# Kernel optimization log

Hardware: AMD Instinct MI355X
Metric: run time of the kernel (lower is better)

The kernel has to match this reference:

```python
import math
import jax
import jax.numpy as jnp
import numpy as np

B = 4096        # number of contexts / segments
T = 262144      # total objects across all segments (avg 64 per segment)
F = 128         # object_size
H = 256         # hidden_size
C = 512         # context_size


def setup_inputs() -> dict:
    key = jax.random.key(0)
    ks = jax.random.split(key, 8)
    objects = jax.random.normal(ks[0], (T, F), dtype=jnp.float32)
    context = jax.random.normal(ks[1], (B, C), dtype=jnp.float32)
    # sorted segment ids; guarantee every segment non-empty by seeding one id per segment
    extra = jax.random.randint(ks[2], (T - B,), 0, B)
    segment_ids = jnp.sort(jnp.concatenate([jnp.arange(B, dtype=extra.dtype), extra])).astype(jnp.int32)
    s = 0.05
    return {
        "objects": objects,
        "context": context,
        "segment_ids": segment_ids,
        "W1": jax.random.normal(ks[3], (F, H), dtype=jnp.float32) * s,
        "b1": jnp.zeros((H,), dtype=jnp.float32),
        "W2": jax.random.normal(ks[4], (H, H), dtype=jnp.float32) * s,
        "b2": jnp.zeros((H,), dtype=jnp.float32),
        "W3": jax.random.normal(ks[5], (H, 2 * H), dtype=jnp.float32) * s,
        "b3": jnp.zeros((2 * H,), dtype=jnp.float32),
        "Wq": jax.random.normal(ks[6], (C, H), dtype=jnp.float32) * s,
        "bq": jnp.zeros((H,), dtype=jnp.float32),
    }


def reference(objects, context, segment_ids, W1, b1, W2, b2, W3, b3, Wq, bq):
    num_segments = context.shape[0]
    # kv MLP: Linear -> ReLU -> Linear -> ReLU -> Linear(2H)
    h = jax.nn.relu(objects @ W1 + b1)
    h = jax.nn.relu(h @ W2 + b2)
    kv = h @ W3 + b3                                   # [T, 2H]
    k, v = jnp.split(kv, 2, axis=1)                    # [T, H] each
    # query per object via repeat_interleave == gather by segment id
    q = (context @ Wq + bq)[segment_ids]               # [T, H]
    logits = jnp.sum(q * k, axis=1) / math.sqrt(k.shape[1])   # [T]
    # per-segment stable softmax
    m = jax.ops.segment_max(logits, segment_ids, num_segments=num_segments)
    e = jnp.exp(logits - m[segment_ids])
    z = jax.ops.segment_sum(e, segment_ids, num_segments=num_segments)
    w = e / z[segment_ids]                             # [T]
    # per-segment weighted sum of values
    embedding = jax.ops.segment_sum(w[:, None] * v, segment_ids, num_segments=num_segments)  # [B, H]
    return embedding, w
```

## Files before the change

kernel.cpp:

```cpp
#include <hip/hip_runtime.h>
#include <hip/hip_bf16.h>

#define T_TOTAL 262144
#define B_SEG   4096

typedef __attribute__((ext_vector_type(8))) short short8;
typedef __attribute__((ext_vector_type(4))) float f32x4;

__device__ __forceinline__ short f2bf(float x) {
    __hip_bfloat16 h = __float2bfloat16(x);
    return *reinterpret_cast<short*>(&h);
}
__device__ __forceinline__ float bf2f(short s) {
    unsigned u = ((unsigned)(unsigned short)s) << 16;
    return __uint_as_float(u);
}

__global__ __launch_bounds__(256) void transpose_weights(
    const float* __restrict__ W1, const float* __restrict__ W2,
    const float* __restrict__ W3,
    short* __restrict__ W1T, short* __restrict__ W2T, short* __restrict__ W3vT) {
    __shared__ float t[64][68];
    const int b = blockIdx.x, tid = threadIdx.x;
    const float* src; short* dst;
    int k0, n0_src, n0_dst, sstride, dstride;
    if (b < 8) {
        int kt = b >> 2, nt = b & 3;
        src = W1; dst = W1T; sstride = 256; dstride = 128;
        k0 = kt * 64; n0_src = nt * 64; n0_dst = nt * 64;
    } else if (b < 24) {
        int id = b - 8, kt = id >> 2, nt = id & 3;
        src = W2; dst = W2T; sstride = 256; dstride = 256;
        k0 = kt * 64; n0_src = nt * 64; n0_dst = nt * 64;
    } else {
        int id = b - 24, kt = id >> 2, nt = id & 3;
        src = W3; dst = W3vT; sstride = 512; dstride = 256;
        k0 = kt * 64; n0_src = 256 + nt * 64; n0_dst = nt * 64;
    }
    {
        int r = tid >> 4, c4 = (tid & 15) * 4;
#pragma unroll
        for (int p = 0; p < 4; p++) {
            int k = p * 16 + r;
            float4 v = *reinterpret_cast<const float4*>(&src[(size_t)(k0 + k) * sstride + n0_src + c4]);
            *reinterpret_cast<float4*>(&t[k][c4]) = v;
        }
    }
    __syncthreads();
    {
        int n = tid >> 2, kq = tid & 3;
        short8 s0, s1;
#pragma unroll
        for (int i = 0; i < 8; i++) s0[i] = f2bf(t[kq * 16 + i][n]);
#pragma unroll
        for (int i = 0; i < 8; i++) s1[i] = f2bf(t[kq * 16 + 8 + i][n]);
        short* o = &dst[(size_t)(n0_dst + n) * dstride + k0 + kq * 16];
        *reinterpret_cast<short8*>(o) = s0;
        *reinterpret_cast<short8*>(o + 8) = s1;
    }
}

__global__ __launch_bounds__(256) void vec_kernel(
    const float* __restrict__ Wq, const float* __restrict__ W3,
    const float* __restrict__ bq, const float* __restrict__ b3,
    float* __restrict__ bz, float* __restrict__ wc, float* __restrict__ c0) {
    const int tid = threadIdx.x;
    if (blockIdx.x == 0) {
        float s = 0.f;
        for (int n = 0; n < 256; n += 4) {
            float4 a = *reinterpret_cast<const float4*>(&W3[(size_t)tid * 512 + n]);
            float4 b = *reinterpret_cast<const float4*>(&bq[n]);
            s += a.x * b.x + a.y * b.y + a.z * b.z + a.w * b.w;
        }
        bz[tid] = s;
    } else {
#pragma unroll
        for (int h = 0; h < 2; h++) {
            int c = h * 256 + tid;
            float s = 0.f;
            for (int n = 0; n < 256; n += 4) {
                float4 a = *reinterpret_cast<const float4*>(&Wq[(size_t)c * 256 + n]);
                float4 b = *reinterpret_cast<const float4*>(&b3[n]);
                s += a.x * b.x + a.y * b.y + a.z * b.z + a.w * b.w;
            }
            wc[c] = s;
        }
        if (tid == 0) {
            float s = 0.f;
            for (int n = 0; n < 256; n++) s += bq[n] * b3[n];
            c0[0] = s;
        }
    }
}

__global__ __launch_bounds__(256) void prep_wqz(
    const float* __restrict__ Wq, const float* __restrict__ W3,
    float* __restrict__ Wqz) {
    __shared__ float wq[16][260];
    __shared__ float w3[16][260];
    const int tid = threadIdx.x;
    const int c0 = (blockIdx.x >> 4) * 16, j0 = (blockIdx.x & 15) * 16;
    {
        int r = tid >> 4, nq = tid & 15;
#pragma unroll
        for (int p = 0; p < 4; p++) {
            int col = nq * 4 + p * 64;
            *reinterpret_cast<float4*>(&wq[r][col]) =
                *reinterpret_cast<const float4*>(&Wq[(size_t)(c0 + r) * 256 + col]);
            *reinterpret_cast<float4*>(&w3[r][col]) =
                *reinterpret_cast<const float4*>(&W3[(size_t)(j0 + r) * 512 + col]);
        }
    }
    __syncthreads();
    const int ci = tid >> 4, ji = tid & 15;
    float s = 0.f;
    for (int n = 0; n < 256; n += 4) {
        float4 a = *reinterpret_cast<const float4*>(&wq[ci][n]);
        float4 b = *reinterpret_cast<const float4*>(&w3[ji][n]);
        s += a.x * b.x + a.y * b.y + a.z * b.z + a.w * b.w;
    }
    Wqz[(size_t)(c0 + ci) * 256 + j0 + ji] = s;
}

__global__ __launch_bounds__(256) void zq_kernel(
    const float* __restrict__ ctx, const float* __restrict__ Wqz,
    const float* __restrict__ bz, float* __restrict__ zq) {
    __shared__ float As[2][16][68];
    const int tid = threadIdx.x;
    const int tm = tid & 15, tn = tid >> 4;
    const int row0 = blockIdx.x * 64, col0 = blockIdx.y * 64;
    const int lr = tid >> 2, lk = tid & 3;

    float acc[4][4];
#pragma unroll
    for (int i = 0; i < 4; i++)
#pragma unroll
        for (int j = 0; j < 4; j++) acc[i][j] = 0.f;

    float4 av = *reinterpret_cast<const float4*>(&ctx[(size_t)(row0 + lr) * 512 + lk * 4]);
    for (int c = 0; c < 32; c++) {
        int cur = c & 1;
        As[cur][lk * 4 + 0][lr] = av.x;
        As[cur][lk * 4 + 1][lr] = av.y;
        As[cur][lk * 4 + 2][lr] = av.z;
        As[cur][lk * 4 + 3][lr] = av.w;
        __syncthreads();
        if (c < 31)
            av = *reinterpret_cast<const float4*>(
                &ctx[(size_t)(row0 + lr) * 512 + (c + 1) * 16 + lk * 4]);
#pragma unroll
        for (int k = 0; k < 16; k++) {
            float4 a = *reinterpret_cast<const float4*>(&As[cur][k][tm * 4]);
            float4 b = *reinterpret_cast<const float4*>(
                &Wqz[(size_t)(c * 16 + k) * 256 + col0 + tn * 4]);
#pragma unroll
            for (int i = 0; i < 4; i++) {
                float ai = (i == 0) ? a.x : (i == 1) ? a.y : (i == 2) ? a.z : a.w;
                acc[i][0] += ai * b.x; acc[i][1] += ai * b.y;
                acc[i][2] += ai * b.z; acc[i][3] += ai * b.w;
            }
        }
    }
    float4 bv = *reinterpret_cast<const float4*>(&bz[col0 + tn * 4]);
#pragma unroll
    for (int i = 0; i < 4; i++) {
        float4 o = {acc[i][0] + bv.x, acc[i][1] + bv.y, acc[i][2] + bv.z, acc[i][3] + bv.w};
        *reinterpret_cast<float4*>(&zq[(size_t)(row0 + tm * 4 + i) * 256 + col0 + tn * 4]) = o;
    }
}

__global__ __launch_bounds__(256) void cvec_kernel(
    const float* __restrict__ ctx, const float* __restrict__ wc,
    const float* __restrict__ c0, float* __restrict__ cbuf) {
    const int tid = threadIdx.x;
    const int row = blockIdx.x * 32 + (tid >> 3);
    const int l = tid & 7;
    float s = 0.f;
    for (int i = 0; i < 64; i += 4) {
        float4 a = *reinterpret_cast<const float4*>(&ctx[(size_t)row * 512 + l * 64 + i]);
        float4 b = *reinterpret_cast<const float4*>(&wc[l * 64 + i]);
        s += a.x * b.x + a.y * b.y + a.z * b.z + a.w * b.w;
    }
    s += __shfl_xor(s, 1); s += __shfl_xor(s, 2); s += __shfl_xor(s, 4);
    if (l == 0) cbuf[row] = s + c0[0];
}

template <int K>
__device__ __forceinline__ void run_layer(
    const short* __restrict__ act, const short* __restrict__ Wt,
    int mbase, int nbase, int l16, int quad, f32x4 acc[4][4]) {
    constexpr int KK = K / 32;
    const f32x4 zero = {0.f, 0.f, 0.f, 0.f};
#pragma unroll
    for (int i = 0; i < 4; i++)
#pragma unroll
        for (int j = 0; j < 4; j++) acc[i][j] = zero;

    int woff[4];
#pragma unroll
    for (int ns = 0; ns < 4; ns++)
        woff[ns] = ((nbase + ns * 16 + l16) * K + quad * 8) * 2;
    const int abase = (mbase + l16) * K * 2;
    const char* actc = reinterpret_cast<const char*>(act);
    const char* wtc  = reinterpret_cast<const char*>(Wt);

    short8 wbuf[2][4];
    short8 areg[4];

#pragma unroll
    for (int ns = 0; ns < 4; ns++)
        wbuf[0][ns] = *reinterpret_cast<const short8*>(wtc + woff[ns]);

#pragma unroll
    for (int kk = 0; kk < KK; kk++) {
        if (kk + 1 < KK) {
#pragma unroll
            for (int ns = 0; ns < 4; ns++)
                wbuf[(kk + 1) & 1][ns] = *reinterpret_cast<const short8*>(
                    wtc + woff[ns] + (kk + 1) * 64);
        }
        {
            const int sg = (((kk * 4 + quad) ^ l16) * 16);
#pragma unroll
            for (int ms = 0; ms < 4; ms++)
                areg[ms] = *reinterpret_cast<const short8*>(
                    actc + abase + ms * 16 * K * 2 + sg);
        }
        const int cb = kk & 1;
#pragma unroll
        for (int ms = 0; ms < 4; ms++)
#pragma unroll
            for (int ns = 0; ns < 4; ns++)
                acc[ms][ns] = __builtin_amdgcn_mfma_f32_16x16x32_bf16(
                    wbuf[cb][ns], areg[ms], acc[ms][ns], 0, 0, 0);
    }
}

__global__ __launch_bounds__(512, 4) void mlp_kernel(
    const float* __restrict__ objects, const int* __restrict__ seg_ids,
    const short* __restrict__ W1T, const short* __restrict__ W2T,
    const short* __restrict__ W3vT,
    const float* __restrict__ b1, const float* __restrict__ b2,
    const float* __restrict__ b3,
    const float* __restrict__ zqbuf, const float* __restrict__ cbuf,
    float* __restrict__ logits_out, short* __restrict__ vout) {
    __shared__ __align__(16) short bufH[128 * 256];
    __shared__ float slots[4][128];

    const int tid  = threadIdx.x;
    const int wave = tid >> 6;
    const int lane = tid & 63;
    const int quad = lane >> 4;
    const int l16  = lane & 15;
    const int mbase = (wave & 1) * 64;
    const int wn    = wave >> 1;
    const int nbase = wn * 64;
    const int row0  = blockIdx.x * 128;

    {
        const float4* op = reinterpret_cast<const float4*>(objects + (size_t)row0 * 128);
#pragma unroll
        for (int i = 0; i < 4; i++) {
            int u = tid + i * 512;
            int m = u >> 4, kg = u & 15;
            float4 x0 = op[u * 2];
            float4 x1 = op[u * 2 + 1];
            short8 s;
            s[0] = f2bf(x0.x); s[1] = f2bf(x0.y); s[2] = f2bf(x0.z); s[3] = f2bf(x0.w);
            s[4] = f2bf(x1.x); s[5] = f2bf(x1.y); s[6] = f2bf(x1.z); s[7] = f2bf(x1.w);
            *reinterpret_cast<short8*>(&bufH[m * 128 + ((kg ^ (m & 15)) * 8)]) = s;
        }
    }
    __syncthreads();

    f32x4 acc[4][4];

    auto store_act = [&](const float* __restrict__ bias) {
#pragma unroll
        for (int ns = 0; ns < 4; ns++) {
            int n0 = nbase + ns * 16 + quad * 4;
            float4 bv = *reinterpret_cast<const float4*>(&bias[n0]);
#pragma unroll
            for (int ms = 0; ms < 4; ms++) {
                int m = mbase + ms * 16 + l16;
                short4 s;
                s.x = f2bf(fmaxf(acc[ms][ns][0] + bv.x, 0.f));
                s.y = f2bf(fmaxf(acc[ms][ns][1] + bv.y, 0.f));
                s.z = f2bf(fmaxf(acc[ms][ns][2] + bv.z, 0.f));
                s.w = f2bf(fmaxf(acc[ms][ns][3] + bv.w, 0.f));
                *reinterpret_cast<short4*>(
                    &bufH[m * 256 + (((n0 >> 3) ^ (m & 15)) * 8) + (n0 & 7)]) = s;
            }
        }
    };

    run_layer<128>(bufH, W1T, mbase, nbase, l16, quad, acc);
    __syncthreads();
    store_act(b1);
    __syncthreads();

    run_layer<256>(bufH, W2T, mbase, nbase, l16, quad, acc);
    __syncthreads();
    {
        float part[4] = {0.f, 0.f, 0.f, 0.f};
        int segm[4];
#pragma unroll
        for (int ms = 0; ms < 4; ms++) segm[ms] = seg_ids[row0 + mbase + ms * 16 + l16];
#pragma unroll
        for (int ns = 0; ns < 4; ns++) {
            int n0 = nbase + ns * 16 + quad * 4;
            float4 bv = *reinterpret_cast<const float4*>(&b2[n0]);
#pragma unroll
            for (int ms = 0; ms < 4; ms++) {
                int m = mbase + ms * 16 + l16;
                float h0 = fmaxf(acc[ms][ns][0] + bv.x, 0.f);
                float h1v = fmaxf(acc[ms][ns][1] + bv.y, 0.f);
                float h2v = fmaxf(acc[ms][ns][2] + bv.z, 0.f);
                float h3 = fmaxf(acc[ms][ns][3] + bv.w, 0.f);
                short4 s;
                s.x = f2bf(h0); s.y = f2bf(h1v); s.z = f2bf(h2v); s.w = f2bf(h3);
                *reinterpret_cast<short4*>(
                    &bufH[m * 256 + (((n0 >> 3) ^ (m & 15)) * 8) + (n0 & 7)]) = s;
                float4 zq4 = *reinterpret_cast<const float4*>(
                    &zqbuf[(size_t)segm[ms] * 256 + n0]);
                part[ms] += h0 * zq4.x + h1v * zq4.y + h2v * zq4.z + h3 * zq4.w;
            }
        }
#pragma unroll
        for (int ms = 0; ms < 4; ms++) {
            float p = part[ms];
            p += __shfl_xor(p, 16);
            p += __shfl_xor(p, 32);
            if (quad == 0) slots[wn][mbase + ms * 16 + l16] = p;
        }
    }
    __syncthreads();
    if (tid < 128) {
        int seg = seg_ids[row0 + tid];
        float s = slots[0][tid] + slots[1][tid] + slots[2][tid] + slots[3][tid] + cbuf[seg];
        logits_out[row0 + tid] = s * 0.0625f;
    }

    run_layer<256>(bufH, W3vT, mbase, nbase, l16, quad, acc);
    __syncthreads();
#pragma unroll
    for (int ns = 0; ns < 4; ns++) {
        int n0 = nbase + ns * 16 + quad * 4;
        float4 bv = *reinterpret_cast<const float4*>(&b3[256 + n0]);
#pragma unroll
        for (int ms = 0; ms < 4; ms++) {
            int m = mbase + ms * 16 + l16;
            short4 s;
            s.x = f2bf(acc[ms][ns][0] + bv.x);
            s.y = f2bf(acc[ms][ns][1] + bv.y);
            s.z = f2bf(acc[ms][ns][2] + bv.z);
            s.w = f2bf(acc[ms][ns][3] + bv.w);
            *reinterpret_cast<short4*>(
                &bufH[m * 256 + (((n0 >> 3) ^ (m & 15)) * 8) + (n0 & 7)]) = s;
        }
    }
    __syncthreads();
#pragma unroll
    for (int i = 0; i < 8; i++) {
        int idx = tid + i * 512;
        int m = idx >> 5, sg = idx & 31;
        short8 val = *reinterpret_cast<const short8*>(&bufH[m * 256 + sg * 8]);
        int n0 = (sg ^ (m & 15)) * 8;
        *reinterpret_cast<short8*>(&vout[(size_t)(row0 + m) * 256 + n0]) = val;
    }
}

__global__ __launch_bounds__(256) void segment_kernel(
    const float* __restrict__ logits, const short* __restrict__ vbuf,
    const int* __restrict__ seg_ids, float* __restrict__ emb,
    float* __restrict__ wout) {
    const int b = blockIdx.x;
    const int tid = threadIdx.x;
    __shared__ int range[2];
    __shared__ float wred[4];
    __shared__ float slots[4][256];

    if (tid < 2) {
        int target = b + tid;
        int lo = 0, hi = T_TOTAL;
        while (lo < hi) {
            int mid = (lo + hi) >> 1;
            if (seg_ids[mid] < target) lo = mid + 1; else hi = mid;
        }
        range[tid] = lo;
    }
    __syncthreads();
    const int start = range[0], end = range[1];

    float mx = -1e30f;
    for (int t = start + tid; t < end; t += 256) mx = fmaxf(mx, logits[t]);
#pragma unroll
    for (int off = 32; off >= 1; off >>= 1) mx = fmaxf(mx, __shfl_xor(mx, off));
    if ((tid & 63) == 0) wred[tid >> 6] = mx;
    __syncthreads();
    mx = fmaxf(fmaxf(wred[0], wred[1]), fmaxf(wred[2], wred[3]));
    __syncthreads();

    float s = 0.f;
    for (int t = start + tid; t < end; t += 256) s += __expf(logits[t] - mx);
#pragma unroll
    for (int off = 32; off >= 1; off >>= 1) s += __shfl_xor(s, off);
    if ((tid & 63) == 0) wred[tid >> 6] = s;
    __syncthreads();
    float invz = 1.f / (wred[0] + wred[1] + wred[2] + wred[3]);

    for (int t = start + tid; t < end; t += 256)
        wout[t] = __expf(logits[t] - mx) * invz;

    const int cg = tid & 63, r = tid >> 6;
    float a0 = 0.f, a1 = 0.f, a2 = 0.f, a3 = 0.f;
    for (int t = start + r; t < end; t += 4) {
        float wv = __expf(logits[t] - mx) * invz;
        short4 v4 = *reinterpret_cast<const short4*>(&vbuf[(size_t)t * 256 + cg * 4]);
        a0 += wv * bf2f(v4.x);
        a1 += wv * bf2f(v4.y);
        a2 += wv * bf2f(v4.z);
        a3 += wv * bf2f(v4.w);
    }
    float4 av = {a0, a1, a2, a3};
    *reinterpret_cast<float4*>(&slots[r][cg * 4]) = av;
    __syncthreads();
    emb[(size_t)b * 256 + tid] =
        slots[0][tid] + slots[1][tid] + slots[2][tid] + slots[3][tid];
}

extern "C" void kernel_launch(void* const* d_in, const int* in_sizes, int n_in,
                              void* d_out, int out_size, void* d_ws, size_t ws_size,
                              hipStream_t stream) {
    const float* objects = (const float*)d_in[0];
    const float* context = (const float*)d_in[1];
    const int*   seg     = (const int*)d_in[2];
    const float* W1 = (const float*)d_in[3];
    const float* b1 = (const float*)d_in[4];
    const float* W2 = (const float*)d_in[5];
    const float* b2 = (const float*)d_in[6];
    const float* W3 = (const float*)d_in[7];
    const float* b3 = (const float*)d_in[8];
    const float* Wq = (const float*)d_in[9];
    const float* bq = (const float*)d_in[10];

    char* ws = (char*)d_ws;
    float* zqbuf = (float*)(ws);
    float* cbuf  = (float*)(ws + 4194304);
    short* W1T   = (short*)(ws + 4210688);
    short* W2T   = (short*)(ws + 4276224);
    short* W3vT  = (short*)(ws + 4407296);
    char*  lreg   = ws + 4538368;
    float* logits = (float*)lreg;
    float* Wqz    = (float*)lreg;
    float* bz     = (float*)(lreg + 524288);
    float* wc     = (float*)(lreg + 525312);
    float* c0     = (float*)(lreg + 527360);
    short* vbuf   = (short*)(ws + 5586944);

    float* emb  = (float*)d_out;
    float* wout = emb + (size_t)B_SEG * 256;

    transpose_weights<<<40, 256, 0, stream>>>(W1, W2, W3, W1T, W2T, W3vT);
    vec_kernel<<<2, 256, 0, stream>>>(Wq, W3, bq, b3, bz, wc, c0);
    prep_wqz<<<512, 256, 0, stream>>>(Wq, W3, Wqz);
    zq_kernel<<<dim3(64, 4), 256, 0, stream>>>(context, Wqz, bz, zqbuf);
    cvec_kernel<<<128, 256, 0, stream>>>(context, wc, c0, cbuf);
    mlp_kernel<<<T_TOTAL / 128, 512, 0, stream>>>(objects, seg, W1T, W2T, W3vT,
                                                  b1, b2, b3, zqbuf, cbuf,
                                                  logits, vbuf);
    segment_kernel<<<B_SEG, 256, 0, stream>>>(logits, vbuf, seg, emb, wout);
}
```

Baseline: 486.1 us.

## Shrink MLP tile to 64 rows, precompute segment starts, use one-wave segment reduction

The MLP kernel now processes 64 rows per 256-thread block instead of 128 rows per 512-thread block, halving the LDS buffer so more blocks fit per CU. The activation loads are moved ahead of the weight prefetch. A new kernel computes segment start offsets once, replacing the per-block binary search. The segment kernel becomes a single wave with multiple accumulators, which removes the LDS reductions and barriers. seg_starts reuses the cbuf workspace region, but it is written after mlp_kernel has consumed cbuf, so the ordering is safe.

```diff
diff --git a/kernel.cpp b/kernel.cpp
--- a/kernel.cpp
+++ b/kernel.cpp
@@ -188,7 +188,7 @@
 template <int K>
 __device__ __forceinline__ void run_layer(
     const short* __restrict__ act, const short* __restrict__ Wt,
-    int mbase, int nbase, int l16, int quad, f32x4 acc[4][4]) {
+    int nbase, int l16, int quad, f32x4 acc[4][4]) {
     constexpr int KK = K / 32;
     const f32x4 zero = {0.f, 0.f, 0.f, 0.f};
 #pragma unroll
@@ -200,7 +200,7 @@
 #pragma unroll
     for (int ns = 0; ns < 4; ns++)
         woff[ns] = ((nbase + ns * 16 + l16) * K + quad * 8) * 2;
-    const int abase = (mbase + l16) * K * 2;
+    const int abase = l16 * K * 2;
     const char* actc = reinterpret_cast<const char*>(act);
     const char* wtc  = reinterpret_cast<const char*>(Wt);
 
@@ -213,19 +213,19 @@
 
 #pragma unroll
     for (int kk = 0; kk < KK; kk++) {
+        {
+            const int sg = (((kk * 4 + quad) ^ l16) * 16);
+#pragma unroll
+            for (int ms = 0; ms < 4; ms++)
+                areg[ms] = *reinterpret_cast<const short8*>(
+                    actc + abase + ms * 16 * K * 2 + sg);
+        }
         if (kk + 1 < KK) {
 #pragma unroll
             for (int ns = 0; ns < 4; ns++)
                 wbuf[(kk + 1) & 1][ns] = *reinterpret_cast<const short8*>(
                     wtc + woff[ns] + (kk + 1) * 64);
         }
-        {
-            const int sg = (((kk * 4 + quad) ^ l16) * 16);
-#pragma unroll
-            for (int ms = 0; ms < 4; ms++)
-                areg[ms] = *reinterpret_cast<const short8*>(
-                    actc + abase + ms * 16 * K * 2 + sg);
-        }
         const int cb = kk & 1;
 #pragma unroll
         for (int ms = 0; ms < 4; ms++)
@@ -236,7 +236,7 @@
     }
 }
 
-__global__ __launch_bounds__(512, 4) void mlp_kernel(
+__global__ __launch_bounds__(256, 4) void mlp_kernel(
     const float* __restrict__ objects, const int* __restrict__ seg_ids,
     const short* __restrict__ W1T, const short* __restrict__ W2T,
     const short* __restrict__ W3vT,
@@ -244,24 +244,22 @@
     const float* __restrict__ b3,
     const float* __restrict__ zqbuf, const float* __restrict__ cbuf,
     float* __restrict__ logits_out, short* __restrict__ vout) {
-    __shared__ __align__(16) short bufH[128 * 256];
-    __shared__ float slots[4][128];
+    __shared__ __align__(16) short bufH[64 * 256];
+    __shared__ float slots[4][64];
 
     const int tid  = threadIdx.x;
     const int wave = tid >> 6;
     const int lane = tid & 63;
     const int quad = lane >> 4;
     const int l16  = lane & 15;
-    const int mbase = (wave & 1) * 64;
-    const int wn    = wave >> 1;
-    const int nbase = wn * 64;
-    const int row0  = blockIdx.x * 128;
+    const int nbase = wave * 64;
+    const int row0  = blockIdx.x * 64;
 
     {
         const float4* op = reinterpret_cast<const float4*>(objects + (size_t)row0 * 128);
 #pragma unroll
         for (int i = 0; i < 4; i++) {
-            int u = tid + i * 512;
+            int u = tid + i * 256;
             int m = u >> 4, kg = u & 15;
             float4 x0 = op[u * 2];
             float4 x1 = op[u * 2 + 1];
@@ -282,7 +280,7 @@
             float4 bv = *reinterpret_cast<const float4*>(&bias[n0]);
 #pragma unroll
             for (int ms = 0; ms < 4; ms++) {
-                int m = mbase + ms * 16 + l16;
+                int m = ms * 16 + l16;
                 short4 s;
                 s.x = f2bf(fmaxf(acc[ms][ns][0] + bv.x, 0.f));
                 s.y = f2bf(fmaxf(acc[ms][ns][1] + bv.y, 0.f));
@@ -294,25 +292,25 @@
         }
     };
 
-    run_layer<128>(bufH, W1T, mbase, nbase, l16, quad, acc);
+    run_layer<128>(bufH, W1T, nbase, l16, quad, acc);
     __syncthreads();
     store_act(b1);
     __syncthreads();
 
-    run_layer<256>(bufH, W2T, mbase, nbase, l16, quad, acc);
+    run_layer<256>(bufH, W2T, nbase, l16, quad, acc);
     __syncthreads();
     {
         float part[4] = {0.f, 0.f, 0.f, 0.f};
         int segm[4];
 #pragma unroll
-        for (int ms = 0; ms < 4; ms++) segm[ms] = seg_ids[row0 + mbase + ms * 16 + l16];
+        for (int ms = 0; ms < 4; ms++) segm[ms] = seg_ids[row0 + ms * 16 + l16];
 #pragma unroll
         for (int ns = 0; ns < 4; ns++) {
             int n0 = nbase + ns * 16 + quad * 4;
             float4 bv = *reinterpret_cast<const float4*>(&b2[n0]);
 #pragma unroll
             for (int ms = 0; ms < 4; ms++) {
-                int m = mbase + ms * 16 + l16;
+                int m = ms * 16 + l16;
                 float h0 = fmaxf(acc[ms][ns][0] + bv.x, 0.f);
                 float h1v = fmaxf(acc[ms][ns][1] + bv.y, 0.f);
                 float h2v = fmaxf(acc[ms][ns][2] + bv.z, 0.f);
@@ -331,17 +329,17 @@
             float p = part[ms];
             p += __shfl_xor(p, 16);
             p += __shfl_xor(p, 32);
-            if (quad == 0) slots[wn][mbase + ms * 16 + l16] = p;
-        }
-    }
-    __syncthreads();
-    if (tid < 128) {
+            if (quad == 0) slots[wave][ms * 16 + l16] = p;
+        }
+    }
+    __syncthreads();
+    if (tid < 64) {
         int seg = seg_ids[row0 + tid];
         float s = slots[0][tid] + slots[1][tid] + slots[2][tid] + slots[3][tid] + cbuf[seg];
         logits_out[row0 + tid] = s * 0.0625f;
     }
 
-    run_layer<256>(bufH, W3vT, mbase, nbase, l16, quad, acc);
+    run_layer<256>(bufH, W3vT, nbase, l16, quad, acc);
     __syncthreads();
 #pragma unroll
     for (int ns = 0; ns < 4; ns++) {
@@ -349,7 +347,7 @@
         float4 bv = *reinterpret_cast<const float4*>(&b3[256 + n0]);
 #pragma unroll
         for (int ms = 0; ms < 4; ms++) {
-            int m = mbase + ms * 16 + l16;
+            int m = ms * 16 + l16;
             short4 s;
             s.x = f2bf(acc[ms][ns][0] + bv.x);
             s.y = f2bf(acc[ms][ns][1] + bv.y);
@@ -362,7 +360,7 @@
     __syncthreads();
 #pragma unroll
     for (int i = 0; i < 8; i++) {
-        int idx = tid + i * 512;
+        int idx = tid + i * 256;
         int m = idx >> 5, sg = idx & 31;
         short8 val = *reinterpret_cast<const short8*>(&bufH[m * 256 + sg * 8]);
         int n0 = (sg ^ (m & 15)) * 8;
@@ -370,63 +368,76 @@
     }
 }
 
-__global__ __launch_bounds__(256) void segment_kernel(
+__global__ __launch_bounds__(256) void seg_starts_kernel(
+    const int* __restrict__ seg, int* __restrict__ starts) {
+    int t = blockIdx.x * 256 + threadIdx.x;
+    if (t >= T_TOTAL) return;
+    int s = seg[t];
+    if (t == 0) {
+        for (int q = 0; q <= s; q++) starts[q] = 0;
+    } else {
+        int p = seg[t - 1];
+        for (int q = p + 1; q <= s; q++) starts[q] = t;
+    }
+}
+
+__global__ __launch_bounds__(64) void segment_kernel(
     const float* __restrict__ logits, const short* __restrict__ vbuf,
-    const int* __restrict__ seg_ids, float* __restrict__ emb,
+    const int* __restrict__ starts, float* __restrict__ emb,
     float* __restrict__ wout) {
     const int b = blockIdx.x;
-    const int tid = threadIdx.x;
-    __shared__ int range[2];
-    __shared__ float wred[4];
-    __shared__ float slots[4][256];
-
-    if (tid < 2) {
-        int target = b + tid;
-        int lo = 0, hi = T_TOTAL;
-        while (lo < hi) {
-            int mid = (lo + hi) >> 1;
-            if (seg_ids[mid] < target) lo = mid + 1; else hi = mid;
-        }
-        range[tid] = lo;
-    }
-    __syncthreads();
-    const int start = range[0], end = range[1];
+    const int lane = threadIdx.x;
+    const int start = starts[b];
+    const int end = (b == B_SEG - 1) ? T_TOTAL : starts[b + 1];
 
     float mx = -1e30f;
-    for (int t = start + tid; t < end; t += 256) mx = fmaxf(mx, logits[t]);
+    for (int t = start + lane; t < end; t += 64) mx = fmaxf(mx, logits[t]);
 #pragma unroll
     for (int off = 32; off >= 1; off >>= 1) mx = fmaxf(mx, __shfl_xor(mx, off));
-    if ((tid & 63) == 0) wred[tid >> 6] = mx;
-    __syncthreads();
-    mx = fmaxf(fmaxf(wred[0], wred[1]), fmaxf(wred[2], wred[3]));
-    __syncthreads();
 
     float s = 0.f;
-    for (int t = start + tid; t < end; t += 256) s += __expf(logits[t] - mx);
+    for (int t = start + lane; t < end; t += 64) s += __expf(logits[t] - mx);
 #pragma unroll
     for (int off = 32; off >= 1; off >>= 1) s += __shfl_xor(s, off);
-    if ((tid & 63) == 0) wred[tid >> 6] = s;
-    __syncthreads();
-    float invz = 1.f / (wred[0] + wred[1] + wred[2] + wred[3]);
-
-    for (int t = start + tid; t < end; t += 256)
+    const float invz = 1.f / s;
+
+    for (int t = start + lane; t < end; t += 64)
         wout[t] = __expf(logits[t] - mx) * invz;
 
-    const int cg = tid & 63, r = tid >> 6;
-    float a0 = 0.f, a1 = 0.f, a2 = 0.f, a3 = 0.f;
-    for (int t = start + r; t < end; t += 4) {
+    float a[4][4];
+#pragma unroll
+    for (int i = 0; i < 4; i++)
+#pragma unroll
+        for (int j = 0; j < 4; j++) a[i][j] = 0.f;
+
+    int t = start;
+    for (; t + 8 <= end; t += 8) {
+#pragma unroll
+        for (int u = 0; u < 8; u++) {
+            float wv = __expf(logits[t + u] - mx) * invz;
+            short4 v4 = *reinterpret_cast<const short4*>(
+                &vbuf[(size_t)(t + u) * 256 + lane * 4]);
+            a[u & 3][0] += wv * bf2f(v4.x);
+            a[u & 3][1] += wv * bf2f(v4.y);
+            a[u & 3][2] += wv * bf2f(v4.z);
+            a[u & 3][3] += wv * bf2f(v4.w);
+        }
+    }
+    for (; t < end; t++) {
         float wv = __expf(logits[t] - mx) * invz;
-        short4 v4 = *reinterpret_cast<const short4*>(&vbuf[(size_t)t * 256 + cg * 4]);
-        a0 += wv * bf2f(v4.x);
-        a1 += wv * bf2f(v4.y);
-        a2 += wv * bf2f(v4.z);
-        a3 += wv * bf2f(v4.w);
-    }
-    float4 av = {a0, a1, a2, a3};
-    *reinterpret_cast<float4*>(&slots[r][cg * 4]) = av;
-    __syncthreads();
-    emb[(size_t)b * 256 + tid] =
-        slots[0][tid] + slots[1][tid] + slots[2][tid] + slots[3][tid];
+        short4 v4 = *reinterpret_cast<const short4*>(
+            &vbuf[(size_t)t * 256 + lane * 4]);
+        a[0][0] += wv * bf2f(v4.x);
+        a[0][1] += wv * bf2f(v4.y);
+        a[0][2] += wv * bf2f(v4.z);
+        a[0][3] += wv * bf2f(v4.w);
+    }
+    float4 o;
+    o.x = a[0][0] + a[1][0] + a[2][0] + a[3][0];
+    o.y = a[0][1] + a[1][1] + a[2][1] + a[3][1];
+    o.z = a[0][2] + a[1][2] + a[2][2] + a[3][2];
+    o.w = a[0][3] + a[1][3] + a[2][3] + a[3][3];
+    *reinterpret_cast<float4*>(&emb[(size_t)b * 256 + lane * 4]) = o;
 }
 
 extern "C" void kernel_launch(void* const* d_in, const int* in_sizes, int n_in,
@@ -447,6 +458,7 @@
     char* ws = (char*)d_ws;
     float* zqbuf = (float*)(ws);
     float* cbuf  = (float*)(ws + 4194304);
+    int*   seg_starts = (int*)(ws + 4194304);
     short* W1T   = (short*)(ws + 4210688);
     short* W2T   = (short*)(ws + 4276224);
     short* W3vT  = (short*)(ws + 4407296);
@@ -466,8 +478,9 @@
     prep_wqz<<<512, 256, 0, stream>>>(Wq, W3, Wqz);
     zq_kernel<<<dim3(64, 4), 256, 0, stream>>>(context, Wqz, bz, zqbuf);
     cvec_kernel<<<128, 256, 0, stream>>>(context, wc, c0, cbuf);
-    mlp_kernel<<<T_TOTAL / 128, 512, 0, stream>>>(objects, seg, W1T, W2T, W3vT,
-                                                  b1, b2, b3, zqbuf, cbuf,
-                                                  logits, vbuf);
-    segment_kernel<<<B_SEG, 256, 0, stream>>>(logits, vbuf, seg, emb, wout);
-}
+    mlp_kernel<<<T_TOTAL / 64, 256, 0, stream>>>(objects, seg, W1T, W2T, W3vT,
+                                                 b1, b2, b3, zqbuf, cbuf,
+                                                 logits, vbuf);
+    seg_starts_kernel<<<T_TOTAL / 256, 256, 0, stream>>>(seg, seg_starts);
+    segment_kernel<<<B_SEG, 64, 0, stream>>>(logits, vbuf, seg_starts, emb, wout);
+}
```

New measurement: 482.7 us. No clear change (-0.7%).
